# Kernel optimization log

Measured on AMD Instinct MI355X. Metric: run time of the kernel, lower is better.

The kernel has to match this reference:

```python
import jax, jax.numpy as jnp
import numpy as np
from jax.scipy.linalg import expm

N, T, IN, C, M = 64, 2048, 8, 2, 10  # batch, time, input_size, channels, hidden_size


def setup_inputs() -> dict:
    key = jax.random.key(0)
    k1, k2 = jax.random.split(key)
    x = jax.random.normal(k1, (N, T, IN), dtype=jnp.float32)
    # Lie-algebra generator parameters; small init keeps expm well-conditioned
    A = jax.random.normal(k2, (C, IN, M, M), dtype=jnp.float32) * (1.0 / (M * IN))
    return {"x": x, "A": A}


def dyadic_prod(X):
    # X: (N, T, C, m, m) -> cumulative (ordered) matrix product over time: (N, C, m, m)
    n, t, c, m, _ = X.shape
    levels = int(np.ceil(np.log2(t)))
    I = jnp.broadcast_to(jnp.eye(m, dtype=X.dtype), (n, 1, c, m, m))
    for _ in range(levels):
        if X.shape[1] % 2 == 1:
            X = jnp.concatenate([X, I], axis=1)  # pad with identity
        Xp = X.reshape(n, -1, 2, c, m, m)
        X = jnp.einsum('ntcij,ntcjk->ntcik', Xp[:, :, 0], Xp[:, :, 1])
    return X[:, 0]


def reference(x, A):
    # Skew-symmetrize generators -> so(m) Lie algebra elements, per channel/input dim
    skew = A - jnp.swapaxes(A, -1, -2)          # (C, IN, m, m)
    dX = x[:, 1:] - x[:, :-1]                   # (N, T-1, IN) path increments
    G = jnp.einsum('nti,cijk->ntcjk', dX, skew) # (N, T-1, C, m, m)
    Mexp = expm(G)                              # batched matrix exponential -> SO(m)
    return dyadic_prod(Mexp)                    # (N, C, m, m)
```

## Files before the change

### kernel.cpp

```cpp
#include <hip/hip_runtime.h>

#define NB     64
#define TT     2048
#define INQ    8
#define CC     2
#define MM     10
#define ROWP   12
#define MATS   124
#define PSTR   20
#define SLEN   8
#define SEGS   64
#define NCHUNK 4
#define NCHAIN (NB*CC)

typedef float v2f __attribute__((ext_vector_type(2)));

__device__ __forceinline__ constexpr int triIdx(int k, int j) {
    return k * 10 + j - ((k + 1) * (k + 2)) / 2;
}

template <int SRC>
__device__ __forceinline__ float dpp_qbcast(float v) {
    const int i = __float_as_int(v);
    const int r = __builtin_amdgcn_update_dpp(i, i, SRC * 0x55, 0xF, 0xF, true);
    return __int_as_float(r);
}

__device__ __forceinline__ void trow_pk(const float* __restrict__ Tri,
                                        v2f* A, v2f* R, const v2f* S, float cj) {
    v2f t[MM];
    t[0] = -S[1] * Tri[triIdx(0, 1)];
    #pragma unroll
    for (int j = 1; j < MM; ++j) t[j] = S[0] * Tri[triIdx(0, j)];
    #pragma unroll
    for (int k = 1; k < MM; ++k) {
        const v2f a = S[k];
        #pragma unroll
        for (int j = 0; j < MM; ++j) {
            if (k == j) continue;
            if (j == 0 && k == 1) continue;
            if (j > k) t[j] += a * Tri[triIdx(k, j)];
            else       t[j] -= a * Tri[triIdx(j, k)];
        }
    }
    #pragma unroll
    for (int j = 0; j < MM; ++j) { A[j] = t[j]; R[j] += cj * t[j]; }
}

__device__ __forceinline__ void trow_s(const float* __restrict__ Tri,
                                       float* A, float* R, const float* S, float cj) {
    float t[MM];
    t[0] = -S[1] * Tri[triIdx(0, 1)];
    #pragma unroll
    for (int j = 1; j < MM; ++j) t[j] = S[0] * Tri[triIdx(0, j)];
    #pragma unroll
    for (int k = 1; k < MM; ++k) {
        const float a = S[k];
        #pragma unroll
        for (int j = 0; j < MM; ++j) {
            if (k == j) continue;
            if (j == 0 && k == 1) continue;
            if (j > k) t[j] += a * Tri[triIdx(k, j)];
            else       t[j] -= a * Tri[triIdx(j, k)];
        }
    }
    #pragma unroll
    for (int j = 0; j < MM; ++j) { A[j] = t[j]; R[j] += cj * t[j]; }
}

__device__ __forceinline__ void pair_combine(float* buf_s, int ls, int rs, int pq) {
    float lrow[5][MM];
    #pragma unroll
    for (int r = 0; r < 5; ++r) {
        const float4* lr = reinterpret_cast<const float4*>(
            &buf_s[ls * MATS + (pq * 5 + r) * ROWP]);
        const float4 a = lr[0], b = lr[1], c4 = lr[2];
        lrow[r][0] = a.x;  lrow[r][1] = a.y;  lrow[r][2] = a.z;  lrow[r][3] = a.w;
        lrow[r][4] = b.x;  lrow[r][5] = b.y;  lrow[r][6] = b.z;  lrow[r][7] = b.w;
        lrow[r][8] = c4.x; lrow[r][9] = c4.y;
    }
    float d[5][MM];
    #pragma unroll
    for (int r = 0; r < 5; ++r)
        #pragma unroll
        for (int j = 0; j < MM; ++j)
            d[r][j] = 0.0f;
    #pragma unroll
    for (int k = 0; k < MM; ++k) {
        const float4* rr = reinterpret_cast<const float4*>(&buf_s[rs * MATS + k * ROWP]);
        const float4 a = rr[0], b = rr[1], c4 = rr[2];
        float rrow[MM];
        rrow[0] = a.x;  rrow[1] = a.y;  rrow[2] = a.z;  rrow[3] = a.w;
        rrow[4] = b.x;  rrow[5] = b.y;  rrow[6] = b.z;  rrow[7] = b.w;
        rrow[8] = c4.x; rrow[9] = c4.y;
        #pragma unroll
        for (int r = 0; r < 5; ++r) {
            const float lv = lrow[r][k];
            #pragma unroll
            for (int j = 0; j < MM; ++j)
                d[r][j] += lv * rrow[j];
        }
    }
    float* dst = &buf_s[ls * MATS + pq * 5 * ROWP];
    #pragma unroll
    for (int r = 0; r < 5; ++r) {
        float4* drow = reinterpret_cast<float4*>(dst + r * ROWP);
        drow[0] = make_float4(d[r][0], d[r][1], d[r][2], d[r][3]);
        drow[1] = make_float4(d[r][4], d[r][5], d[r][6], d[r][7]);
        drow[2] = make_float4(d[r][8], d[r][9], 0.0f, 0.0f);
    }
}

__global__ __launch_bounds__(256)
void dev_serial(const float* __restrict__ x,
                const float* __restrict__ A,
                float* __restrict__ ws)
{
    __shared__ __align__(16) float skp_s[24 * PSTR];
    __shared__ __align__(16) float buf_s[SEGS * MATS];

    const int tid   = threadIdx.x;
    const int chain = blockIdx.x >> 2;
    const int qt    = blockIdx.x & 3;
    const int n     = chain >> 1;
    const int c     = chain & 1;

    for (int e = tid; e < 24 * 16; e += 256) {
        const int p   = e >> 4;
        const int rem = e & 15;
        const int ip  = rem >> 1;
        const int h   = rem & 1;
        const int t   = 2 * p + h;
        float v = 0.0f;
        if (t < 45) {
            int k = 0, r2 = t;
            while (r2 >= 9 - k) { r2 -= (9 - k); ++k; }
            const int j = k + 1 + r2;
            const float* Ab = A + (size_t)(c * INQ + ip) * (MM * MM);
            v = Ab[k * MM + j] - Ab[j * MM + k];
        }
        skp_s[p * PSTR + 2 * ip + h] = v;
    }
    for (int p = tid; p < 24; p += 256) {
        skp_s[p * PSTR + 16] = 0.0f; skp_s[p * PSTR + 17] = 0.0f;
        skp_s[p * PSTR + 18] = 0.0f; skp_s[p * PSTR + 19] = 0.0f;
    }
    __syncthreads();

    const int seg = tid >> 2;
    const int q   = tid & 3;
    const int p0  = (q < 2) ? 3 * q : (q == 2 ? 6 : 8);
    const int sr  = (q < 2) ? (3 * q + 2) : 9;
    const bool hasS = (q < 2);

    v2f   R01[MM];
    float R2[MM];
    #pragma unroll
    for (int j = 0; j < MM; ++j) {
        R01[j] = (v2f){ (j == p0) ? 1.0f : 0.0f, (j == p0 + 1) ? 1.0f : 0.0f };
        R2[j]  = (j == sr) ? 1.0f : 0.0f;
    }

    const float* xb = x + (size_t)n * TT * INQ;
    const int t0 = qt * (SEGS * SLEN) + seg * SLEN;

    float4 cur0, cur1, nxt0, nxt1;
    {
        const float4* p = reinterpret_cast<const float4*>(xb + (size_t)t0 * INQ);
        cur0 = p[0]; cur1 = p[1];
        int t1 = t0 + 1; if (t1 > TT - 1) t1 = TT - 1;
        const float4* pn = reinterpret_cast<const float4*>(xb + (size_t)t1 * INQ);
        nxt0 = pn[0]; nxt1 = pn[1];
    }

    #pragma unroll 1
    for (int s = 0; s < SLEN; ++s) {
        float dx[INQ];
        dx[0] = nxt0.x - cur0.x; dx[1] = nxt0.y - cur0.y;
        dx[2] = nxt0.z - cur0.z; dx[3] = nxt0.w - cur0.w;
        dx[4] = nxt1.x - cur1.x; dx[5] = nxt1.y - cur1.y;
        dx[6] = nxt1.z - cur1.z; dx[7] = nxt1.w - cur1.w;
        cur0 = nxt0; cur1 = nxt1;
        {
            int t2 = t0 + s + 2; if (t2 > TT - 1) t2 = TT - 1;
            const float4* pn = reinterpret_cast<const float4*>(xb + (size_t)t2 * INQ);
            nxt0 = pn[0]; nxt1 = pn[1];
        }

        v2f tvp[6];
        #pragma unroll
        for (int pp = 0; pp < 6; ++pp) {
            const v2f* sp = reinterpret_cast<const v2f*>(&skp_s[(6 * q + pp) * PSTR]);
            v2f acc = dx[0] * sp[0];
            #pragma unroll
            for (int ip = 1; ip < INQ; ++ip)
                acc += dx[ip] * sp[ip];
            tvp[pp] = acc;
        }
        float tv[12];
        #pragma unroll
        for (int pp = 0; pp < 6; ++pp) { tv[2 * pp] = tvp[pp].x; tv[2 * pp + 1] = tvp[pp].y; }

        float Tri[45];
        #define TRIFILL(U) Tri[U] = dpp_qbcast<(U) / 12>(tv[(U) % 12]);
        TRIFILL(0)  TRIFILL(1)  TRIFILL(2)  TRIFILL(3)  TRIFILL(4)
        TRIFILL(5)  TRIFILL(6)  TRIFILL(7)  TRIFILL(8)  TRIFILL(9)
        TRIFILL(10) TRIFILL(11) TRIFILL(12) TRIFILL(13) TRIFILL(14)
        TRIFILL(15) TRIFILL(16) TRIFILL(17) TRIFILL(18) TRIFILL(19)
        TRIFILL(20) TRIFILL(21) TRIFILL(22) TRIFILL(23) TRIFILL(24)
        TRIFILL(25) TRIFILL(26) TRIFILL(27) TRIFILL(28) TRIFILL(29)
        TRIFILL(30) TRIFILL(31) TRIFILL(32) TRIFILL(33) TRIFILL(34)
        TRIFILL(35) TRIFILL(36) TRIFILL(37) TRIFILL(38) TRIFILL(39)
        TRIFILL(40) TRIFILL(41) TRIFILL(42) TRIFILL(43) TRIFILL(44)
        #undef TRIFILL

        v2f   A01[MM];
        float A2[MM];
        trow_pk(Tri, A01, R01, R01, 1.0f);
        trow_s (Tri, A2,  R2,  R2,  1.0f);
        trow_pk(Tri, A01, R01, A01, 0.5f);
        trow_s (Tri, A2,  R2,  A2,  0.5f);
        trow_pk(Tri, A01, R01, A01, 0.16666667f);
        trow_s (Tri, A2,  R2,  A2,  0.16666667f);
        trow_pk(Tri, A01, R01, A01, 0.041666668f);
        trow_s (Tri, A2,  R2,  A2,  0.041666668f);
        trow_pk(Tri, A01, R01, A01, 0.0083333338f);
        trow_s (Tri, A2,  R2,  A2,  0.0083333338f);
    }

    {
        float* dst = &buf_s[seg * MATS];
        float4* d0 = reinterpret_cast<float4*>(dst + p0 * ROWP);
        d0[0] = make_float4(R01[0].x, R01[1].x, R01[2].x, R01[3].x);
        d0[1] = make_float4(R01[4].x, R01[5].x, R01[6].x, R01[7].x);
        d0[2] = make_float4(R01[8].x, R01[9].x, 0.0f, 0.0f);
        float4* d1 = reinterpret_cast<float4*>(dst + (p0 + 1) * ROWP);
        d1[0] = make_float4(R01[0].y, R01[1].y, R01[2].y, R01[3].y);
        d1[1] = make_float4(R01[4].y, R01[5].y, R01[6].y, R01[7].y);
        d1[2] = make_float4(R01[8].y, R01[9].y, 0.0f, 0.0f);
        if (hasS) {
            float4* d2 = reinterpret_cast<float4*>(dst + sr * ROWP);
            d2[0] = make_float4(R2[0], R2[1], R2[2], R2[3]);
            d2[1] = make_float4(R2[4], R2[5], R2[6], R2[7]);
            d2[2] = make_float4(R2[8], R2[9], 0.0f, 0.0f);
        }
    }
    __syncthreads();

    #pragma unroll 1
    for (int span = 2; span <= SEGS; span <<= 1) {
        const int np = SEGS / span;
        if (tid < 2 * np) {
            const int pr = tid >> 1;
            const int pq = tid & 1;
            pair_combine(buf_s, pr * span, pr * span + (span >> 1), pq);
        }
        __syncthreads();
    }

    if (tid < 30) {
        const float4 v = reinterpret_cast<const float4*>(buf_s)[tid];
        reinterpret_cast<float4*>(ws)[((size_t)chain * NCHUNK + qt) * 30 + tid] = v;
    }
}

__global__ __launch_bounds__(256)
void dev_tree4(const float* __restrict__ ws, float* __restrict__ out)
{
    __shared__ __align__(16) float buf_s[4 * MATS];
    const int tid   = threadIdx.x;
    const int chain = blockIdx.x;

    if (tid < 120) {
        const int m  = tid / 30;
        const int o4 = tid - m * 30;
        const float4 v = reinterpret_cast<const float4*>(ws)[((size_t)chain * 4 + m) * 30 + o4];
        reinterpret_cast<float4*>(&buf_s[m * MATS])[o4] = v;
    }
    __syncthreads();

    if (tid < 4)
        pair_combine(buf_s, (tid >> 1) * 2, (tid >> 1) * 2 + 1, tid & 1);
    __syncthreads();
    if (tid < 2)
        pair_combine(buf_s, 0, 2, tid);
    __syncthreads();

    if (tid < 100) {
        const int i = tid / 10;
        const int j = tid - i * 10;
        out[(size_t)chain * 100 + tid] = buf_s[i * ROWP + j];
    }
}

extern "C" void kernel_launch(void* const* d_in, const int* in_sizes, int n_in,
                              void* d_out, int out_size, void* d_ws, size_t ws_size,
                              hipStream_t stream) {
    (void)in_sizes; (void)n_in; (void)out_size; (void)ws_size;
    const float* x = (const float*)d_in[0];
    const float* A = (const float*)d_in[1];
    float* out = (float*)d_out;
    float* ws  = (float*)d_ws;

    dev_serial<<<dim3(NCHAIN * NCHUNK), dim3(256), 0, stream>>>(x, A, ws);
    dev_tree4<<<dim3(NCHAIN), dim3(256), 0, stream>>>(ws, out);
}
```

Measured before the change: 109.4 us.

## Fuse final chunk reduction into serial kernel via last-block atomic counter

Removes the second kernel launch that combined the four per-chain chunk products. Each block now bumps a global atomic counter after writing its partial matrix, and the last block to finish multiplies all chunks for every chain, with 256 threads each handling half a matrix. This saves a launch and its gap but adds a memset launch and puts the whole final reduction on a single block. The ws layout is the same as before (120 floats per chunk).

```diff
diff --git a/kernel.cpp b/kernel.cpp
--- a/kernel.cpp
+++ b/kernel.cpp
@@ -12,6 +12,9 @@
 #define SEGS   64
 #define NCHUNK 4
 #define NCHAIN (NB*CC)
+#define NBLK   (NCHAIN*NCHUNK)
+#define WSMAT  120
+#define CTRO   (NBLK*WSMAT)
 
 typedef float v2f __attribute__((ext_vector_type(2)));
 
@@ -114,10 +117,12 @@
 __global__ __launch_bounds__(256)
 void dev_serial(const float* __restrict__ x,
                 const float* __restrict__ A,
-                float* __restrict__ ws)
+                float* __restrict__ ws,
+                float* __restrict__ out)
 {
     __shared__ __align__(16) float skp_s[24 * PSTR];
     __shared__ __align__(16) float buf_s[SEGS * MATS];
+    __shared__ int last_s;
 
     const int tid   = threadIdx.x;
     const int chain = blockIdx.x >> 2;
@@ -262,34 +267,69 @@
         const float4 v = reinterpret_cast<const float4*>(buf_s)[tid];
         reinterpret_cast<float4*>(ws)[((size_t)chain * NCHUNK + qt) * 30 + tid] = v;
     }
-}
-
-__global__ __launch_bounds__(256)
-void dev_tree4(const float* __restrict__ ws, float* __restrict__ out)
-{
-    __shared__ __align__(16) float buf_s[4 * MATS];
-    const int tid   = threadIdx.x;
-    const int chain = blockIdx.x;
-
-    if (tid < 120) {
-        const int m  = tid / 30;
-        const int o4 = tid - m * 30;
-        const float4 v = reinterpret_cast<const float4*>(ws)[((size_t)chain * 4 + m) * 30 + o4];
-        reinterpret_cast<float4*>(&buf_s[m * MATS])[o4] = v;
-    }
     __syncthreads();
 
-    if (tid < 4)
-        pair_combine(buf_s, (tid >> 1) * 2, (tid >> 1) * 2 + 1, tid & 1);
+    unsigned int* ctr = reinterpret_cast<unsigned int*>(ws + CTRO);
+    if (tid == 0) {
+        __threadfence();
+        const unsigned int old = atomicAdd(ctr, 1u);
+        last_s = (old == NBLK - 1) ? 1 : 0;
+    }
     __syncthreads();
-    if (tid < 2)
-        pair_combine(buf_s, 0, 2, tid);
-    __syncthreads();
-
-    if (tid < 100) {
-        const int i = tid / 10;
-        const int j = tid - i * 10;
-        out[(size_t)chain * 100 + tid] = buf_s[i * ROWP + j];
+    if (last_s) {
+        __threadfence();
+        const int ch = tid >> 1;
+        const int pq = tid & 1;
+        const float* base = ws + (size_t)ch * NCHUNK * WSMAT;
+
+        float Rr[5][MM];
+        #pragma unroll
+        for (int r = 0; r < 5; ++r) {
+            const float4* lr = reinterpret_cast<const float4*>(
+                base + (pq * 5 + r) * ROWP);
+            const float4 a = lr[0], b = lr[1], c4 = lr[2];
+            Rr[r][0] = a.x;  Rr[r][1] = a.y;  Rr[r][2] = a.z;  Rr[r][3] = a.w;
+            Rr[r][4] = b.x;  Rr[r][5] = b.y;  Rr[r][6] = b.z;  Rr[r][7] = b.w;
+            Rr[r][8] = c4.x; Rr[r][9] = c4.y;
+        }
+
+        #pragma unroll 1
+        for (int ck = 1; ck < NCHUNK; ++ck) {
+            const float* B = base + ck * WSMAT;
+            float d[5][MM];
+            #pragma unroll
+            for (int r = 0; r < 5; ++r)
+                #pragma unroll
+                for (int j = 0; j < MM; ++j)
+                    d[r][j] = 0.0f;
+            #pragma unroll
+            for (int k = 0; k < MM; ++k) {
+                const float4* br = reinterpret_cast<const float4*>(B + k * ROWP);
+                const float4 a = br[0], b = br[1], c4 = br[2];
+                float brow[MM];
+                brow[0] = a.x;  brow[1] = a.y;  brow[2] = a.z;  brow[3] = a.w;
+                brow[4] = b.x;  brow[5] = b.y;  brow[6] = b.z;  brow[7] = b.w;
+                brow[8] = c4.x; brow[9] = c4.y;
+                #pragma unroll
+                for (int r = 0; r < 5; ++r) {
+                    const float rv = Rr[r][k];
+                    #pragma unroll
+                    for (int j = 0; j < MM; ++j)
+                        d[r][j] += rv * brow[j];
+                }
+            }
+            #pragma unroll
+            for (int r = 0; r < 5; ++r)
+                #pragma unroll
+                for (int j = 0; j < MM; ++j)
+                    Rr[r][j] = d[r][j];
+        }
+
+        #pragma unroll
+        for (int r = 0; r < 5; ++r)
+            #pragma unroll
+            for (int j = 0; j < MM; ++j)
+                out[(size_t)ch * 100 + (pq * 5 + r) * 10 + j] = Rr[r][j];
     }
 }
 
@@ -302,6 +342,6 @@
     float* out = (float*)d_out;
     float* ws  = (float*)d_ws;
 
-    dev_serial<<<dim3(NCHAIN * NCHUNK), dim3(256), 0, stream>>>(x, A, ws);
-    dev_tree4<<<dim3(NCHAIN), dim3(256), 0, stream>>>(ws, out);
-}
+    hipMemsetAsync((char*)d_ws + CTRO * sizeof(float), 0, sizeof(unsigned int), stream);
+    dev_serial<<<dim3(NBLK), dim3(256), 0, stream>>>(x, A, ws, out);
+}
```

New measurement: 124.5 us. 1.14x slower.
